# Kernel optimization log

Hardware: AMD Instinct MI355X
Metric: run time of the kernel (lower is better)

The kernel has to match this reference:

```python
import jax, jax.numpy as jnp
import numpy as np

E = 2048            # total edges in the batch
L = 8               # num_features == max_walk_length
G = 128             # num_graphs in the batch
HID = 128
N_NODES = 4096


def setup_inputs() -> dict:
    key = jax.random.key(0)
    k0, k1, k2, k3 = jax.random.split(key, 4)
    edge_index = jax.random.randint(k0, (2, E), 0, N_NODES, dtype=jnp.int32)
    edge_graph = jnp.sort(jax.random.randint(k1, (E,), 0, G, dtype=jnp.int32))
    W1 = jax.random.normal(k2, (L, HID), dtype=jnp.float32) * (1.0 / np.sqrt(L))
    b1 = jnp.zeros((HID,), dtype=jnp.float32)
    W2 = jax.random.normal(k3, (HID, 1), dtype=jnp.float32) * (1.0 / np.sqrt(HID))
    b2 = jnp.zeros((1,), dtype=jnp.float32)
    return {"edge_index": edge_index, "edge_graph": edge_graph,
            "W1": W1, "b1": b1, "W2": W2, "b2": b2}


def reference(edge_index, edge_graph, W1, b1, W2, b2):
    src, dst = edge_index[0], edge_index[1]  # edge i = (src_i, dst_i)
    # Non-backtracking edge matrix: B[i, j] = 1 iff dst_j == src_i and src_j != dst_i
    # (matches the python condition `u != l and v == k` with edge_i=(k,l), edge_j=(u,v))
    B = ((dst[None, :] == src[:, None]) & (src[None, :] != dst[:, None])).astype(jnp.float32)
    e = B.shape[0]
    walk_len = W1.shape[0]

    # B^1 .. B^L via scan, collecting diagonals (non-backtracking closed-walk counts per edge)
    def step(P, _):
        P = P @ B
        return P, jnp.diagonal(P)

    _, diags = jax.lax.scan(step, jnp.eye(e, dtype=jnp.float32), None, length=walk_len)
    # diags: [L, E] -> per-graph signatures [G, L]
    sig = jax.ops.segment_sum(diags.T, edge_graph, num_segments=G)

    # MLP (eval mode: dropout is identity)
    h = jax.nn.relu(sig @ W1 + b1)
    return h @ W2 + b2
```

## Files before the change

kernel.cpp:

```cpp
#include <hip/hip_runtime.h>


typedef unsigned long long u64;

constexpr int E_EDGES  = 2048;
constexpr int L_WALK   = 8;
constexpr int G_GRAPHS = 128;
constexpr int HID      = 128;
constexpr int N_NODES  = 4096;
constexpr int TPB      = 1024;
constexpr int CAP      = 2048;
constexpr int NIL      = 0xFFF;

__device__ __forceinline__ void ballot_push(u64 e2, int lane, int* ctr, u64* buf) {
    u64 m = __ballot(1);
    int leader = __ffsll(m) - 1;
    int rank   = __popcll(m & ((1ull << lane) - 1ull));
    int bpos = 0;
    if (lane == leader) bpos = atomicAdd(ctr, (int)__popcll(m));
    bpos = __shfl(bpos, leader);
    if (bpos + rank < CAP) buf[bpos + rank] = e2;
}

__launch_bounds__(TPB, 1)
__global__ void nbc_all(const int* __restrict__ edge_index,
                        const int* __restrict__ edge_graph,
                        const float* __restrict__ W1,
                        const float* __restrict__ b1,
                        const float* __restrict__ W2,
                        const float* __restrict__ b2,
                        float* __restrict__ out)
{
    __shared__ u64 s_bufA[CAP];
    __shared__ u64 s_bufB[CAP];
    __shared__ u64 s_node[E_EDGES];
    __shared__ int s_sig[G_GRAPHS * L_WALK];
    __shared__ int s_nn[L_WALK + 1];
    __shared__ float s_W1[L_WALK * HID];
    __shared__ float s_b1[HID];
    __shared__ float s_W2[HID];
    __shared__ float s_b2;

    int* s_head = (int*)s_bufA;

    const int t    = threadIdx.x;
    const int lane = t & 63;

    const int2 se2 = ((const int2*)edge_index)[t];
    const int2 de2 = ((const int2*)(edge_index + E_EDGES))[t];
    const int2 ge2 = ((const int2*)edge_graph)[t];
    s_W1[t] = W1[t];
    if (t < HID) { s_b1[t] = b1[t]; s_W2[t] = W2[t]; }
    if (t == 0) s_b2 = b2[0];
    s_sig[t] = 0;
    if (t <= L_WALK) s_nn[t] = 0;
    s_head[t] = -1; s_head[t + TPB] = -1;
    s_head[t + 2 * TPB] = -1; s_head[t + 3 * TPB] = -1;
    __syncthreads();

    const int e0 = 2 * t, e1 = 2 * t + 1;
    const int prev0 = atomicExch(&s_head[de2.x], e0);
    const int prev1 = atomicExch(&s_head[de2.y], e1);
    __syncthreads();

    const int h0 = s_head[se2.x] & NIL;
    const int h1 = s_head[se2.y] & NIL;
    s_node[e0] = (u64)se2.x | ((u64)de2.x << 12) | ((u64)h0 << 24)
               | ((u64)(prev0 & NIL) << 36);
    s_node[e1] = (u64)se2.y | ((u64)de2.y << 12) | ((u64)h1 << 24)
               | ((u64)(prev1 & NIL) << 36);
    __syncthreads();

    {
        int p0 = h0, p1 = h1;
        while ((p0 != NIL) | (p1 != NIL)) {
            u64 q0 = (p0 != NIL) ? s_node[p0] : 0;
            u64 q1 = (p1 != NIL) ? s_node[p1] : 0;
            if (p0 != NIL) {
                int sb = (int)(q0 & NIL);
                if (sb != de2.x) {
                    if (p0 == e0) atomicAdd(&s_sig[ge2.x * L_WALK + 0], 1);
                    u64 en = (u64)e0 | (((q0 >> 12) & 0xFFFFFFull) << 11)
                           | ((u64)ge2.x << 35);
                    ballot_push(en, lane, &s_nn[1], s_bufA);
                }
                p0 = (int)((q0 >> 36) & NIL);
            }
            if (p1 != NIL) {
                int sb = (int)(q1 & NIL);
                if (sb != de2.y) {
                    if (p1 == e1) atomicAdd(&s_sig[ge2.y * L_WALK + 0], 1);
                    u64 en = (u64)e1 | (((q1 >> 12) & 0xFFFFFFull) << 11)
                           | ((u64)ge2.y << 35);
                    ballot_push(en, lane, &s_nn[1], s_bufA);
                }
                p1 = (int)((q1 >> 36) & NIL);
            }
        }
    }
    __syncthreads();

    u64* cur = s_bufA;
    u64* nxt = s_bufB;
    for (int d = 1; d < L_WALK; ++d) {
        int n_cur = s_nn[d];
        if (n_cur > CAP) n_cur = CAP;
        for (int idx = t; idx < n_cur; idx += TPB) {
            u64 e = cur[idx];
            int s   = (int)( e        & 0x7FF);
            int dcc = (int)((e >> 11) & NIL);
            int ptr = (int)((e >> 23) & NIL);
            u64 gb  = e & (0x7Full << 35);
            while (ptr != NIL) {
                u64 q = s_node[ptr];
                int sb = (int)(q & NIL);
                int nx = (int)((q >> 36) & NIL);
                if (sb != dcc) {
                    if (ptr == s)
                        atomicAdd(&s_sig[(int)(gb >> 35) * L_WALK + d], 1);
                    if (d < L_WALK - 1) {
                        u64 e2 = (u64)s | (((q >> 12) & 0xFFFFFFull) << 11) | gb;
                        ballot_push(e2, lane, &s_nn[d + 1], nxt);
                    }
                }
                ptr = nx;
            }
        }
        u64* tmp = cur; cur = nxt; nxt = tmp;
        __syncthreads();
    }

    float* s_part = (float*)s_node;
    {
        const int g   = t >> 3;
        const int sub = t & 7;
        float sv[L_WALK];
        #pragma unroll
        for (int k = 0; k < L_WALK; ++k) sv[k] = (float)s_sig[g * L_WALK + k];
        float o = 0.0f;
        const int j0 = sub * 16;
        #pragma unroll 4
        for (int jj = 0; jj < 16; ++jj) {
            int j = j0 + jj;
            float a = s_b1[j];
            #pragma unroll
            for (int k = 0; k < L_WALK; ++k) a += sv[k] * s_W1[k * HID + j];
            o += fmaxf(a, 0.0f) * s_W2[j];
        }
        s_part[t] = o;
    }
    __syncthreads();
    if (t < G_GRAPHS) {
        float r = s_b2;
        #pragma unroll
        for (int s = 0; s < 8; ++s) r += s_part[t * 8 + s];
        out[t] = r;
    }
}

extern "C" void kernel_launch(void* const* d_in, const int* in_sizes, int n_in,
                              void* d_out, int out_size, void* d_ws, size_t ws_size,
                              hipStream_t stream) {
    const int*   edge_index = (const int*)d_in[0];
    const int*   edge_graph = (const int*)d_in[1];
    const float* W1 = (const float*)d_in[2];
    const float* b1 = (const float*)d_in[3];
    const float* W2 = (const float*)d_in[4];
    const float* b2 = (const float*)d_in[5];
    float* out = (float*)d_out;

    nbc_all<<<1, TPB, 0, stream>>>(edge_index, edge_graph, W1, b1, W2, b2, out);
}
```

Before: 73.75 us.

## Use per-wavefront frontier queues to remove block-wide barriers between walk depths

New measurement: 70.63 us. 1.04x faster.

```diff
diff --git a/kernel.cpp b/kernel.cpp
--- a/kernel.cpp
+++ b/kernel.cpp
@@ -7,9 +7,9 @@
 constexpr int L_WALK   = 8;
 constexpr int G_GRAPHS = 128;
 constexpr int HID      = 128;
-constexpr int N_NODES  = 4096;
 constexpr int TPB      = 1024;
-constexpr int CAP      = 2048;
+constexpr int NWAVE    = TPB / 64;
+constexpr int CAPW     = 128;
 constexpr int NIL      = 0xFFF;
 
 __device__ __forceinline__ void ballot_push(u64 e2, int lane, int* ctr, u64* buf) {
@@ -19,7 +19,8 @@
     int bpos = 0;
     if (lane == leader) bpos = atomicAdd(ctr, (int)__popcll(m));
     bpos = __shfl(bpos, leader);
-    if (bpos + rank < CAP) buf[bpos + rank] = e2;
+    int p = bpos + rank;
+    if (p < CAPW) buf[p] = e2;
 }
 
 __launch_bounds__(TPB, 1)
@@ -31,20 +32,20 @@
                         const float* __restrict__ b2,
                         float* __restrict__ out)
 {
-    __shared__ u64 s_bufA[CAP];
-    __shared__ u64 s_bufB[CAP];
+    __shared__ u64 s_buf[NWAVE * 2 * CAPW];
     __shared__ u64 s_node[E_EDGES];
     __shared__ int s_sig[G_GRAPHS * L_WALK];
-    __shared__ int s_nn[L_WALK + 1];
+    __shared__ int s_nn[NWAVE * 12];
     __shared__ float s_W1[L_WALK * HID];
     __shared__ float s_b1[HID];
     __shared__ float s_W2[HID];
     __shared__ float s_b2;
 
-    int* s_head = (int*)s_bufA;
+    int* s_head = (int*)s_buf;
 
     const int t    = threadIdx.x;
     const int lane = t & 63;
+    const int wid  = t >> 6;
 
     const int2 se2 = ((const int2*)edge_index)[t];
     const int2 de2 = ((const int2*)(edge_index + E_EDGES))[t];
@@ -53,7 +54,7 @@
     if (t < HID) { s_b1[t] = b1[t]; s_W2[t] = W2[t]; }
     if (t == 0) s_b2 = b2[0];
     s_sig[t] = 0;
-    if (t <= L_WALK) s_nn[t] = 0;
+    if (t < NWAVE * 12) s_nn[t] = 0;
     s_head[t] = -1; s_head[t + TPB] = -1;
     s_head[t + 2 * TPB] = -1; s_head[t + 3 * TPB] = -1;
     __syncthreads();
@@ -71,6 +72,10 @@
                | ((u64)(prev1 & NIL) << 36);
     __syncthreads();
 
+    int* nn   = s_nn + wid * 12;
+    u64* bufA = s_buf + (size_t)(wid * 2) * CAPW;
+    u64* bufB = bufA + CAPW;
+
     {
         int p0 = h0, p1 = h1;
         while ((p0 != NIL) | (p1 != NIL)) {
@@ -82,7 +87,7 @@
                     if (p0 == e0) atomicAdd(&s_sig[ge2.x * L_WALK + 0], 1);
                     u64 en = (u64)e0 | (((q0 >> 12) & 0xFFFFFFull) << 11)
                            | ((u64)ge2.x << 35);
-                    ballot_push(en, lane, &s_nn[1], s_bufA);
+                    ballot_push(en, lane, &nn[1], bufA);
                 }
                 p0 = (int)((q0 >> 36) & NIL);
             }
@@ -92,20 +97,20 @@
                     if (p1 == e1) atomicAdd(&s_sig[ge2.y * L_WALK + 0], 1);
                     u64 en = (u64)e1 | (((q1 >> 12) & 0xFFFFFFull) << 11)
                            | ((u64)ge2.y << 35);
-                    ballot_push(en, lane, &s_nn[1], s_bufA);
+                    ballot_push(en, lane, &nn[1], bufA);
                 }
                 p1 = (int)((q1 >> 36) & NIL);
             }
         }
     }
-    __syncthreads();
 
-    u64* cur = s_bufA;
-    u64* nxt = s_bufB;
+    u64* cur = bufA;
+    u64* nxt = bufB;
     for (int d = 1; d < L_WALK; ++d) {
-        int n_cur = s_nn[d];
-        if (n_cur > CAP) n_cur = CAP;
-        for (int idx = t; idx < n_cur; idx += TPB) {
+        __threadfence_block();
+        int n_cur = nn[d];
+        if (n_cur > CAPW) n_cur = CAPW;
+        for (int idx = lane; idx < n_cur; idx += 64) {
             u64 e = cur[idx];
             int s   = (int)( e        & 0x7FF);
             int dcc = (int)((e >> 11) & NIL);
@@ -120,15 +125,15 @@
                         atomicAdd(&s_sig[(int)(gb >> 35) * L_WALK + d], 1);
                     if (d < L_WALK - 1) {
                         u64 e2 = (u64)s | (((q >> 12) & 0xFFFFFFull) << 11) | gb;
-                        ballot_push(e2, lane, &s_nn[d + 1], nxt);
+                        ballot_push(e2, lane, &nn[d + 1], nxt);
                     }
                 }
                 ptr = nx;
             }
         }
         u64* tmp = cur; cur = nxt; nxt = tmp;
-        __syncthreads();
     }
+    __syncthreads();
 
     float* s_part = (float*)s_node;
     {
```
